# Performance work log

Measured on AMD Instinct MI355X. Metric: run time of the kernel, lower is better.

Reference implementation:

```python
import jax, jax.numpy as jnp
import numpy as np

COMMITMENT_COST = 0.25


def setup_inputs() -> dict:
    key = jax.random.key(0)
    k1, k2 = jax.random.split(key)
    inputs = jax.random.normal(k1, (32, 64, 64, 64), dtype=jnp.float32)  # b c h w
    num_embeddings, embedding_dim = 1024, 64
    # matches torch uniform_(-1/K, 1/K) init distributionally
    embedding = jax.random.uniform(
        k2, (num_embeddings, embedding_dim), dtype=jnp.float32,
        minval=-1.0 / num_embeddings, maxval=1.0 / num_embeddings)
    return {"inputs": inputs, "embedding": embedding}


def reference(inputs, embedding):
    # b c h w -> b h w c
    x = jnp.transpose(inputs, (0, 2, 3, 1))
    b, h, w, c = x.shape
    flat = x.reshape(-1, c)  # [N, D]
    dists = (jnp.sum(flat * flat, axis=1, keepdims=True)
             + jnp.sum(embedding * embedding, axis=1)
             - 2.0 * flat @ embedding.T)  # [N, K]
    idx = jnp.argmin(dists, axis=1)  # [N]
    quantized = embedding[idx].reshape(b, h, w, c)  # gather == one-hot matmul
    # elementwise MSE losses (reduction='none'); stop-gradient mirrors .detach()
    e_latent = (jax.lax.stop_gradient(quantized) - x) ** 2
    q_latent = (quantized - jax.lax.stop_gradient(x)) ** 2
    loss = q_latent + COMMITMENT_COST * e_latent  # [b, h, w, c]
    # straight-through estimator
    quantized_st = x + jax.lax.stop_gradient(quantized - x)
    quantized_out = jnp.transpose(quantized_st, (0, 3, 1, 2))  # b h w c -> b c h w
    return quantized_out, loss, idx.reshape(b, h, w)
```

## Files before the change

### kernel.cpp

```cpp
#include <hip/hip_runtime.h>

#define NPTS    131072
#define KC      1024
#define DD      64
#define HWSZ    4096
#define MARGINF 6e-5f

typedef __attribute__((ext_vector_type(8))) short short8;
typedef __attribute__((ext_vector_type(4))) float f32x4;

__device__ __forceinline__ ushort bf16_rne(float x) {
    unsigned u = __float_as_uint(x);
    unsigned r = u + 0x7fffu + ((u >> 16) & 1u);
    return (ushort)(r >> 16);
}

__device__ __forceinline__ float np_pairwise64(const float* a) {
#pragma clang fp contract(off)
    float r0 = a[0], r1 = a[1], r2 = a[2], r3 = a[3];
    float r4 = a[4], r5 = a[5], r6 = a[6], r7 = a[7];
    for (int i = 8; i < 64; i += 8) {
        r0 += a[i + 0]; r1 += a[i + 1]; r2 += a[i + 2]; r3 += a[i + 3];
        r4 += a[i + 4]; r5 += a[i + 5]; r6 += a[i + 6]; r7 += a[i + 7];
    }
    return ((r0 + r1) + (r2 + r3)) + ((r4 + r5) + (r6 + r7));
}

__global__ void vq_prep_e(const float* __restrict__ emb, float* __restrict__ se32,
                          float* __restrict__ sebB, ushort* __restrict__ Ebuf) {
    int k = blockIdx.x * blockDim.x + threadIdx.x;
    if (k >= KC) return;
    const float* e = emb + k * DD;
    float sq[DD];
    {
#pragma clang fp contract(off)
        for (int d = 0; d < DD; ++d) sq[d] = e[d] * e[d];
    }
    float s = np_pairwise64(sq);
    se32[k] = s;
    sebB[k] = s + 0.5f;
    const int tile = k >> 4, colk = k & 15;
    for (int d = 0; d < DD; ++d) {
        int kh = d >> 5, quad = (d & 31) >> 3, jj = d & 7;
        float ev = e[d];
        ushort hb = bf16_rne(ev);
        float  hf = __uint_as_float(((unsigned)hb) << 16);
        ushort lb = bf16_rne(ev - hf);
        int pos = (quad * 16 + colk) * 8 + jj;
        Ebuf[((tile * 2 + kh) * 2 + 0) * 512 + pos] = hb;
        Ebuf[((tile * 2 + kh) * 2 + 1) * 512 + pos] = lb;
    }
}

__global__ void __launch_bounds__(256)
vq_main(const float* __restrict__ in, const float* __restrict__ emb,
        const ushort* __restrict__ Ebuf, const float* __restrict__ sebB,
        float* __restrict__ outq, float* __restrict__ outl, float* __restrict__ outi,
        int* __restrict__ cnt, int* __restrict__ queue) {
    __shared__ float xs[64][129];
    __shared__ int   sidx[128];
    const int tid = threadIdx.x;
    const int n0  = blockIdx.x * 128;
    const int b   = n0 >> 12;
    const int hw0 = n0 & 4095;
    const float* inb = in + (size_t)b * DD * HWSZ;

#pragma unroll
    for (int it = 0; it < 32; ++it) {
        int f = tid + it * 256;
        int c = f >> 7, j = f & 127;
        xs[c][j] = inb[c * HWSZ + hw0 + j];
    }
    __syncthreads();

    const int lane = tid & 63, wave = tid >> 6;
    const int quad = lane >> 4, col = lane & 15;

    short8 A[2][2][2];
#pragma unroll
    for (int p = 0; p < 2; ++p) {
        int pt = wave * 32 + p * 16 + col;
#pragma unroll
        for (int kh = 0; kh < 2; ++kh) {
            short8 ah, al;
#pragma unroll
            for (int j = 0; j < 8; ++j) {
                float xv = xs[kh * 32 + quad * 8 + j][pt];
                ushort hb = bf16_rne(xv);
                float  hf = __uint_as_float(((unsigned)hb) << 16);
                ah[j] = (short)hb;
                al[j] = (short)bf16_rne(xv - hf);
            }
            A[p][kh][0] = ah; A[p][kh][1] = al;
        }
    }

    unsigned b1[8], b2[8];
#pragma unroll
    for (int s = 0; s < 8; ++s) { b1[s] = 0xFFFFFFFFu; b2[s] = 0xFFFFFFFFu; }

    for (int g = 0; g < 16; ++g) {
        short8 B[4][2][2];
        float  sB[4];
#pragma unroll
        for (int s = 0; s < 4; ++s) {
            int tile = g * 4 + s;
            sB[s] = sebB[tile * 16 + col];
#pragma unroll
            for (int kh = 0; kh < 2; ++kh)
#pragma unroll
                for (int hl = 0; hl < 2; ++hl)
                    B[s][kh][hl] = *(const short8*)(Ebuf + ((tile * 2 + kh) * 2 + hl) * 512 + lane * 8);
        }
        f32x4 acc[2][4];
#pragma unroll
        for (int p = 0; p < 2; ++p)
#pragma unroll
            for (int s = 0; s < 4; ++s) acc[p][s] = (f32x4){0.f, 0.f, 0.f, 0.f};
#pragma unroll
        for (int p = 0; p < 2; ++p)
#pragma unroll
            for (int s = 0; s < 4; ++s) {
                acc[p][s] = __builtin_amdgcn_mfma_f32_16x16x32_bf16(A[p][0][0], B[s][0][0], acc[p][s], 0, 0, 0);
                acc[p][s] = __builtin_amdgcn_mfma_f32_16x16x32_bf16(A[p][1][0], B[s][1][0], acc[p][s], 0, 0, 0);
                acc[p][s] = __builtin_amdgcn_mfma_f32_16x16x32_bf16(A[p][0][0], B[s][0][1], acc[p][s], 0, 0, 0);
                acc[p][s] = __builtin_amdgcn_mfma_f32_16x16x32_bf16(A[p][1][0], B[s][1][1], acc[p][s], 0, 0, 0);
                acc[p][s] = __builtin_amdgcn_mfma_f32_16x16x32_bf16(A[p][0][1], B[s][0][0], acc[p][s], 0, 0, 0);
                acc[p][s] = __builtin_amdgcn_mfma_f32_16x16x32_bf16(A[p][1][1], B[s][1][0], acc[p][s], 0, 0, 0);
            }
#pragma unroll
        for (int p = 0; p < 2; ++p)
#pragma unroll
            for (int r = 0; r < 4; ++r) {
                unsigned q[4];
#pragma unroll
                for (int s = 0; s < 4; ++s) {
                    float t = fmaf(-2.f, acc[p][s][r], sB[s]);
                    q[s] = (__float_as_uint(t) & 0xFFFFFFC0u) | (unsigned)(g * 4 + s);
                }
                unsigned a  = min(q[0], q[1]), bb = max(q[0], q[1]);
                unsigned c2 = min(q[2], q[3]), d2 = max(q[2], q[3]);
                unsigned lo = min(a, c2), hi = max(a, c2);
                unsigned sec = min(min(bb, d2), hi);
                int sl = p * 4 + r;
                b2[sl] = min(min(b2[sl], sec), max(b1[sl], lo));
                b1[sl] = min(b1[sl], lo);
            }
    }

    unsigned v1[8], v2[8]; int ci[8];
#pragma unroll
    for (int s = 0; s < 8; ++s) {
        ci[s] = (int)(b1[s] & 63u) * 16 + col;
        v1[s] = b1[s] & 0xFFFFFFC0u;
        v2[s] = b2[s] & 0xFFFFFFC0u;
    }
#pragma unroll
    for (int off = 1; off < 16; off <<= 1) {
#pragma unroll
        for (int s = 0; s < 8; ++s) {
            unsigned o1 = (unsigned)__shfl_xor((int)v1[s], off);
            unsigned o2 = (unsigned)__shfl_xor((int)v2[s], off);
            int      oi = __shfl_xor(ci[s], off);
            unsigned nb2 = min(min(v2[s], o2), max(v1[s], o1));
            bool take = (o1 < v1[s]) || (o1 == v1[s] && oi < ci[s]);
            v1[s] = take ? o1 : v1[s];
            ci[s] = take ? oi : ci[s];
            v2[s] = nb2;
        }
    }
#pragma unroll
    for (int s = 0; s < 8; ++s) {
        if (col == s) {
            int jloc = wave * 32 + (s >> 2) * 16 + quad * 4 + (s & 3);
            sidx[jloc] = ci[s];
            float f1 = __uint_as_float(v1[s]), f2 = __uint_as_float(v2[s]);
            if (f2 - f1 < MARGINF) { int pos = atomicAdd(cnt, 1); queue[pos] = n0 + jloc; }
        }
    }
    __syncthreads();

    for (int t = 0; t < 32; ++t) {
        int jloc = wave * 32 + t;
        int kidx = sidx[jloc];
        float qv = emb[kidx * DD + lane];
        float x  = xs[lane][jloc];
        float dv = qv - x;
        float l  = dv * dv;
        outl[(size_t)(n0 + jloc) * DD + lane] = fmaf(0.25f, l, l);
        outq[((size_t)(b * DD) + lane) * HWSZ + hw0 + jloc] = x + (qv - x);
    }
    if (lane < 32) outi[n0 + wave * 32 + lane] = (float)sidx[wave * 32 + lane];
}

__global__ void __launch_bounds__(256)
vq_fix(const float* __restrict__ in, const float* __restrict__ emb,
       const float* __restrict__ se32,
       const int* __restrict__ queue, const int* __restrict__ cnt,
       float* __restrict__ outq, float* __restrict__ outl, float* __restrict__ outi) {
    const int lane = threadIdx.x & 63;
    const int gw   = blockIdx.x * 4 + (threadIdx.x >> 6);
    const int nwav = gridDim.x * 4;
    const int total = *cnt;
    for (int qi = gw; qi < total; qi += nwav) {
        const int n  = queue[qi];
        const int b  = n >> 12, hw = n & 4095;
        const float* inb = in + (size_t)b * DD * HWSZ + hw;
        float x[DD], sq[DD];
        {
#pragma clang fp contract(off)
            for (int d = 0; d < DD; ++d) x[d]  = inb[d * HWSZ];
            for (int d = 0; d < DD; ++d) sq[d] = x[d] * x[d];
        }
        const float sx = np_pairwise64(sq);
        float bD = 3.4e38f; int bi = 0x7fffffff;
        for (int j = 0; j < 16; ++j) {
            int k = lane + (j << 6);
            const float* er = emb + k * DD;
            double acc = 0.0;
#pragma unroll
            for (int d = 0; d < DD; ++d)
                acc = fma((double)x[d], (double)er[d], acc);
            float m2 = (float)(2.0 * acc);
            float s1, Dv;
            {
#pragma clang fp contract(off)
                s1 = sx + se32[k];
                Dv = s1 - m2;
            }
            if (Dv < bD) { bD = Dv; bi = k; }
        }
#pragma unroll
        for (int off = 32; off > 0; off >>= 1) {
            float oD = __shfl_down(bD, off);
            int   oi = __shfl_down(bi, off);
            if (oD < bD || (oD == bD && oi < bi)) { bD = oD; bi = oi; }
        }
        bi = __shfl(bi, 0);
        int old = (int)outi[n];
        if (bi != old) {
            float xv = in[((size_t)b * DD + lane) * HWSZ + hw];
            float qv = emb[bi * DD + lane];
            float dv = qv - xv;
            float l  = dv * dv;
            outl[(size_t)n * DD + lane] = fmaf(0.25f, l, l);
            outq[((size_t)b * DD + lane) * HWSZ + hw] = xv + (qv - xv);
            if (lane == 0) outi[n] = (float)bi;
        }
    }
}

extern "C" void kernel_launch(void* const* d_in, const int* in_sizes, int n_in,
                              void* d_out, int out_size, void* d_ws, size_t ws_size,
                              hipStream_t stream) {
    const float* in  = (const float*)d_in[0];
    const float* emb = (const float*)d_in[1];

    float* outq = (float*)d_out;
    float* outl = outq + (size_t)NPTS * DD;
    float* outi = outl + (size_t)NPTS * DD;

    char*   ws    = (char*)d_ws;
    float*  se32  = (float*)ws;
    float*  sebB  = (float*)(ws + 4096);
    ushort* Ebuf  = (ushort*)(ws + 8192);
    int*    cnt   = (int*)(ws + 8192 + 262144);
    int*    queue = (int*)(ws + 8192 + 262144 + 256);

    hipMemsetAsync(cnt, 0, sizeof(int), stream);
    vq_prep_e<<<4, 256, 0, stream>>>(emb, se32, sebB, Ebuf);
    vq_main<<<NPTS / 128, 256, 0, stream>>>(in, emb, Ebuf, sebB, outq, outl, outi, cnt, queue);
    vq_fix<<<512, 256, 0, stream>>>(in, emb, se32, queue, cnt, outq, outl, outi);
}
```

Measured before the change: 268.7 us.

## Coalesce prep, stage quantized output through LDS, lane-parallel fix distances

The embedding prep kernel now uses 16 blocks. Each block loads 64 codewords into shared memory and then builds the bf16 hi/lo split cooperatively, replacing the old one-thread-per-codeword serial loops. The main kernel writes the straight-through output back into the xs tile and then stores it with fully coalesced row writes instead of strided per-lane stores. The fix kernel now spreads each dot product across lanes in the d dimension, reduces with xor shuffles and scans codewords in order, replacing the per-lane 64-element double FMA chains and the final argmin shuffle. This adds an extra barrier and many shuffles per codeword in the fix path.

```diff
diff --git a/kernel.cpp b/kernel.cpp
--- a/kernel.cpp
+++ b/kernel.cpp
@@ -15,40 +15,50 @@
     return (ushort)(r >> 16);
 }
 
-__device__ __forceinline__ float np_pairwise64(const float* a) {
+__device__ __forceinline__ float np_pairwise64_sq(const float* a) {
 #pragma clang fp contract(off)
-    float r0 = a[0], r1 = a[1], r2 = a[2], r3 = a[3];
-    float r4 = a[4], r5 = a[5], r6 = a[6], r7 = a[7];
+    float r0 = a[0] * a[0], r1 = a[1] * a[1], r2 = a[2] * a[2], r3 = a[3] * a[3];
+    float r4 = a[4] * a[4], r5 = a[5] * a[5], r6 = a[6] * a[6], r7 = a[7] * a[7];
     for (int i = 8; i < 64; i += 8) {
-        r0 += a[i + 0]; r1 += a[i + 1]; r2 += a[i + 2]; r3 += a[i + 3];
-        r4 += a[i + 4]; r5 += a[i + 5]; r6 += a[i + 6]; r7 += a[i + 7];
+        r0 += a[i + 0] * a[i + 0]; r1 += a[i + 1] * a[i + 1];
+        r2 += a[i + 2] * a[i + 2]; r3 += a[i + 3] * a[i + 3];
+        r4 += a[i + 4] * a[i + 4]; r5 += a[i + 5] * a[i + 5];
+        r6 += a[i + 6] * a[i + 6]; r7 += a[i + 7] * a[i + 7];
     }
     return ((r0 + r1) + (r2 + r3)) + ((r4 + r5) + (r6 + r7));
 }
 
-__global__ void vq_prep_e(const float* __restrict__ emb, float* __restrict__ se32,
-                          float* __restrict__ sebB, ushort* __restrict__ Ebuf) {
-    int k = blockIdx.x * blockDim.x + threadIdx.x;
-    if (k >= KC) return;
-    const float* e = emb + k * DD;
-    float sq[DD];
-    {
-#pragma clang fp contract(off)
-        for (int d = 0; d < DD; ++d) sq[d] = e[d] * e[d];
-    }
-    float s = np_pairwise64(sq);
-    se32[k] = s;
-    sebB[k] = s + 0.5f;
-    const int tile = k >> 4, colk = k & 15;
-    for (int d = 0; d < DD; ++d) {
+__global__ void __launch_bounds__(256)
+vq_prep_e(const float* __restrict__ emb, float* __restrict__ se32,
+          float* __restrict__ sebB, ushort* __restrict__ Ebuf) {
+    __shared__ float es_[64][65];
+    const int tid = threadIdx.x;
+    const int k0  = blockIdx.x * 64;
+#pragma unroll
+    for (int it = 0; it < 16; ++it) {
+        int f = tid + it * 256;
+        int kk = f >> 6, d = f & 63;
+        es_[kk][d] = emb[(size_t)(k0 + kk) * DD + d];
+    }
+    __syncthreads();
+    if (tid < 64) {
+        float s = np_pairwise64_sq(&es_[tid][0]);
+        se32[k0 + tid] = s;
+        sebB[k0 + tid] = s + 0.5f;
+    }
+#pragma unroll
+    for (int it = 0; it < 16; ++it) {
+        int f = tid + it * 256;
+        int kk = f >> 6, d = f & 63;
+        int k = k0 + kk;
+        int tile = k >> 4, colk = k & 15;
         int kh = d >> 5, quad = (d & 31) >> 3, jj = d & 7;
-        float ev = e[d];
+        float ev = es_[kk][d];
         ushort hb = bf16_rne(ev);
         float  hf = __uint_as_float(((unsigned)hb) << 16);
-        ushort lb = bf16_rne(ev - hf);
         int pos = (quad * 16 + colk) * 8 + jj;
         Ebuf[((tile * 2 + kh) * 2 + 0) * 512 + pos] = hb;
-        Ebuf[((tile * 2 + kh) * 2 + 1) * 512 + pos] = lb;
+        Ebuf[((tile * 2 + kh) * 2 + 1) * 512 + pos] = bf16_rne(ev - hf);
     }
 }
 
@@ -188,9 +198,16 @@
         float dv = qv - x;
         float l  = dv * dv;
         outl[(size_t)(n0 + jloc) * DD + lane] = fmaf(0.25f, l, l);
-        outq[((size_t)(b * DD) + lane) * HWSZ + hw0 + jloc] = x + (qv - x);
+        xs[lane][jloc] = x + (qv - x);
     }
     if (lane < 32) outi[n0 + wave * 32 + lane] = (float)sidx[wave * 32 + lane];
+    __syncthreads();
+#pragma unroll
+    for (int it = 0; it < 32; ++it) {
+        int f = tid + it * 256;
+        int c = f >> 7, j = f & 127;
+        outq[((size_t)(b * DD) + c) * HWSZ + hw0 + j] = xs[c][j];
+    }
 }
 
 __global__ void __launch_bounds__(256)
@@ -206,45 +223,43 @@
         const int n  = queue[qi];
         const int b  = n >> 12, hw = n & 4095;
         const float* inb = in + (size_t)b * DD * HWSZ + hw;
-        float x[DD], sq[DD];
-        {
+        float x[DD];
+        for (int d = 0; d < DD; ++d) x[d] = inb[d * HWSZ];
+        const float sx = np_pairwise64_sq(x);
+        const double xv = (double)in[((size_t)b * DD + lane) * HWSZ + hw];
+
+        float bD = 3.4e38f; int bi = 0;
+        for (int k0 = 0; k0 < KC; k0 += 4) {
+            double dot[4];
+#pragma unroll
+            for (int u = 0; u < 4; ++u)
+                dot[u] = xv * (double)emb[(size_t)(k0 + u) * DD + lane];
+#pragma unroll
+            for (int off = 32; off > 0; off >>= 1) {
+#pragma unroll
+                for (int u = 0; u < 4; ++u)
+                    dot[u] += __shfl_xor(dot[u], off);
+            }
+#pragma unroll
+            for (int u = 0; u < 4; ++u) {
+                float m2 = (float)(2.0 * dot[u]);
+                float s1, Dv;
+                {
 #pragma clang fp contract(off)
-            for (int d = 0; d < DD; ++d) x[d]  = inb[d * HWSZ];
-            for (int d = 0; d < DD; ++d) sq[d] = x[d] * x[d];
-        }
-        const float sx = np_pairwise64(sq);
-        float bD = 3.4e38f; int bi = 0x7fffffff;
-        for (int j = 0; j < 16; ++j) {
-            int k = lane + (j << 6);
-            const float* er = emb + k * DD;
-            double acc = 0.0;
-#pragma unroll
-            for (int d = 0; d < DD; ++d)
-                acc = fma((double)x[d], (double)er[d], acc);
-            float m2 = (float)(2.0 * acc);
-            float s1, Dv;
-            {
-#pragma clang fp contract(off)
-                s1 = sx + se32[k];
-                Dv = s1 - m2;
-            }
-            if (Dv < bD) { bD = Dv; bi = k; }
-        }
-#pragma unroll
-        for (int off = 32; off > 0; off >>= 1) {
-            float oD = __shfl_down(bD, off);
-            int   oi = __shfl_down(bi, off);
-            if (oD < bD || (oD == bD && oi < bi)) { bD = oD; bi = oi; }
-        }
-        bi = __shfl(bi, 0);
+                    s1 = sx + se32[k0 + u];
+                    Dv = s1 - m2;
+                }
+                if (Dv < bD) { bD = Dv; bi = k0 + u; }
+            }
+        }
         int old = (int)outi[n];
         if (bi != old) {
-            float xv = in[((size_t)b * DD + lane) * HWSZ + hw];
-            float qv = emb[bi * DD + lane];
-            float dv = qv - xv;
-            float l  = dv * dv;
+            float xvf = in[((size_t)b * DD + lane) * HWSZ + hw];
+            float qv  = emb[bi * DD + lane];
+            float dv  = qv - xvf;
+            float l   = dv * dv;
             outl[(size_t)n * DD + lane] = fmaf(0.25f, l, l);
-            outq[((size_t)b * DD + lane) * HWSZ + hw] = xv + (qv - xv);
+            outq[((size_t)b * DD + lane) * HWSZ + hw] = xvf + (qv - xvf);
             if (lane == 0) outi[n] = (float)bi;
         }
     }
@@ -268,7 +283,7 @@
     int*    queue = (int*)(ws + 8192 + 262144 + 256);
 
     hipMemsetAsync(cnt, 0, sizeof(int), stream);
-    vq_prep_e<<<4, 256, 0, stream>>>(emb, se32, sebB, Ebuf);
+    vq_prep_e<<<16, 256, 0, stream>>>(emb, se32, sebB, Ebuf);
     vq_main<<<NPTS / 128, 256, 0, stream>>>(in, emb, Ebuf, sebB, outq, outl, outi, cnt, queue);
     vq_fix<<<512, 256, 0, stream>>>(in, emb, se32, queue, cnt, outq, outl, outi);
 }
```

Measured after the change: 566.9 us. 2.11x slower.
